# Kernel optimization log

Hardware: AMD Instinct MI355X
Metric: run time of the kernel (lower is better)

The kernel has to match this reference:

```python
import jax, jax.numpy as jnp
import numpy as np

N_NODES = 100000
N_EDGES = 1000000
N_GRAPHS = 128
IN_DIM, HID, LAT, N_LAYERS = 32, 64, 32, 3


def setup_inputs() -> dict:
    key = jax.random.key(0)
    ks = jax.random.split(key, 10)
    x = jax.random.normal(ks[0], (N_NODES, IN_DIM), dtype=jnp.float32)
    edge_index = jax.random.randint(ks[1], (2, N_EDGES), 0, N_NODES, dtype=jnp.int64)
    batch = jnp.sort(jax.random.randint(ks[2], (N_NODES,), 0, N_GRAPHS, dtype=jnp.int64))
    s_in = 1.0 / np.sqrt(IN_DIM)
    s_h = 1.0 / np.sqrt(HID)
    return {
        "x": x,
        "edge_index": edge_index,
        "batch": batch,
        "w_in": jax.random.normal(ks[3], (IN_DIM, HID), dtype=jnp.float32) * s_in,
        "b_in": jnp.zeros((HID,), jnp.float32),
        "w1": jax.random.normal(ks[4], (N_LAYERS, HID, HID), dtype=jnp.float32) * s_h,
        "b1": jnp.zeros((N_LAYERS, HID), jnp.float32),
        "w2": jax.random.normal(ks[5], (N_LAYERS, HID, HID), dtype=jnp.float32) * s_h,
        "b2": jnp.zeros((N_LAYERS, HID), jnp.float32),
        "w_fc": jax.random.normal(ks[6], (HID, LAT), dtype=jnp.float32) * s_h,
        "b_fc": jnp.zeros((LAT,), jnp.float32),
    }


def reference(x, edge_index, batch, w_in, b_in, w1, b1, w2, b2, w_fc, b_fc):
    # Input projection: [N, in] -> [N, H]
    h = x @ w_in + b_in
    src, dst = edge_index[0], edge_index[1]
    for i in range(N_LAYERS):
        h_skip = h
        # GINConv (eps=0): aggregate neighbor sum then MLP
        agg = jax.ops.segment_sum(h[src], dst, num_segments=N_NODES)  # [N, H]
        m = h + agg
        m = jax.nn.relu(m @ w1[i] + b1[i])
        m = jax.nn.relu(m @ w2[i] + b2[i])
        # dropout is identity in eval mode; residual skip
        h = m + h_skip
    # global_add_pool over graphs
    pooled = jax.ops.segment_sum(h, batch, num_segments=N_GRAPHS)  # [G, H]
    return pooled @ w_fc + b_fc
```

## Files before the change

kernel.cpp:

```cpp
#include <hip/hip_runtime.h>

#define N_NODES 100000
#define N_EDGES 1000000
#define N_GRAPHS 128
#define IN_DIM 32
#define HID 64
#define LAT 32
#define N_LAYERS 3

#define MPAD 68
#define NB_SUM ((N_NODES + 255) / 256)

__global__ __launch_bounds__(256) void proj_kernel(
    const float* __restrict__ x, const float* __restrict__ w_in,
    const float* __restrict__ b_in, float* __restrict__ h) {
    __shared__ float ws[IN_DIM * HID];
    __shared__ float xs[4 * IN_DIM];
    int tid = threadIdx.x;
    for (int i = tid; i < IN_DIM * HID / 4; i += 256)
        ((float4*)ws)[i] = ((const float4*)w_in)[i];
    if (tid < 32) {
        int r = tid >> 3, c4 = tid & 7;
        int nn = blockIdx.x * 4 + r;
        float4 v = make_float4(0.f, 0.f, 0.f, 0.f);
        if (nn < N_NODES) v = ((const float4*)(x + (size_t)nn * IN_DIM))[c4];
        ((float4*)xs)[tid] = v;
    }
    __syncthreads();
    int w = tid >> 6, j = tid & 63;
    int n = blockIdx.x * 4 + w;
    if (n >= N_NODES) return;
    float acc = b_in[j];
#pragma unroll
    for (int k = 0; k < IN_DIM; k += 4) {
        float4 xv = *(const float4*)&xs[w * IN_DIM + k];
        acc += xv.x * ws[(k + 0) * HID + j];
        acc += xv.y * ws[(k + 1) * HID + j];
        acc += xv.z * ws[(k + 2) * HID + j];
        acc += xv.w * ws[(k + 3) * HID + j];
    }
    h[(size_t)n * HID + j] = acc;
}

__global__ __launch_bounds__(256) void hist_kernel(const int* __restrict__ ei,
                                                   int* __restrict__ counts) {
    int e = blockIdx.x * 256 + threadIdx.x;
    if (e < N_EDGES) atomicAdd(&counts[ei[N_EDGES + e]], 1);
}

__global__ __launch_bounds__(256) void block_sum_kernel(
    const int* __restrict__ counts, int* __restrict__ bsums) {
    __shared__ int sd[4];
    int i = blockIdx.x * 256 + threadIdx.x;
    int v = (i < N_NODES) ? counts[i] : 0;
#pragma unroll
    for (int off = 32; off >= 1; off >>= 1) v += __shfl_down(v, off);
    int lane = threadIdx.x & 63, w = threadIdx.x >> 6;
    if (lane == 0) sd[w] = v;
    __syncthreads();
    if (threadIdx.x == 0) bsums[blockIdx.x] = sd[0] + sd[1] + sd[2] + sd[3];
}

__global__ __launch_bounds__(256) void scan_bsums_kernel(
    const int* __restrict__ bsums, int* __restrict__ bofs, int nb) {
    __shared__ int tmp[256];
    __shared__ int carry;
    int tid = threadIdx.x;
    if (tid == 0) carry = 0;
    __syncthreads();
    for (int base = 0; base < nb; base += 256) {
        int v = (base + tid < nb) ? bsums[base + tid] : 0;
        tmp[tid] = v;
        __syncthreads();
        for (int off = 1; off < 256; off <<= 1) {
            int t = (tid >= off) ? tmp[tid - off] : 0;
            __syncthreads();
            tmp[tid] += t;
            __syncthreads();
        }
        if (base + tid < nb) bofs[base + tid] = carry + tmp[tid] - v;
        __syncthreads();
        if (tid == 255) carry += tmp[255];
        __syncthreads();
    }
}

__global__ __launch_bounds__(256) void offsets_kernel(
    const int* __restrict__ counts, const int* __restrict__ bofs,
    int* __restrict__ offsets, int* __restrict__ cursor) {
    __shared__ int tmp[256];
    int tid = threadIdx.x;
    int i = blockIdx.x * 256 + tid;
    int v = (i < N_NODES) ? counts[i] : 0;
    tmp[tid] = v;
    __syncthreads();
    for (int off = 1; off < 256; off <<= 1) {
        int t = (tid >= off) ? tmp[tid - off] : 0;
        __syncthreads();
        tmp[tid] += t;
        __syncthreads();
    }
    int excl = tmp[tid] - v + bofs[blockIdx.x];
    if (i < N_NODES) {
        offsets[i] = excl;
        cursor[i] = excl;
        if (i == N_NODES - 1) offsets[N_NODES] = excl + v;
    }
}

__global__ __launch_bounds__(256) void fill_kernel(const int* __restrict__ ei,
                                                   int* __restrict__ cursor,
                                                   int* __restrict__ srcs) {
    int e = blockIdx.x * 256 + threadIdx.x;
    if (e < N_EDGES) {
        int d = ei[N_EDGES + e];
        int p = atomicAdd(&cursor[d], 1);
        srcs[p] = ei[e];
    }
}

__global__ __launch_bounds__(256) void gather_kernel(
    const int* __restrict__ offsets, const int* __restrict__ srcs,
    const float* __restrict__ h, float* __restrict__ agg) {
    int w = threadIdx.x >> 6, j = threadIdx.x & 63;
    int n = blockIdx.x * 4 + w;
    if (n >= N_NODES) return;
    int beg = offsets[n], end = offsets[n + 1];
    float acc0 = 0.f, acc1 = 0.f, acc2 = 0.f, acc3 = 0.f;
    for (int c = beg; c < end; c += 64) {
        int myS = (c + j < end) ? srcs[c + j] : 0;
        int m = min(64, end - c);
        int i = 0;
        for (; i + 3 < m; i += 4) {
            int s0 = __shfl(myS, i);
            int s1 = __shfl(myS, i + 1);
            int s2 = __shfl(myS, i + 2);
            int s3 = __shfl(myS, i + 3);
            acc0 += h[(size_t)s0 * HID + j];
            acc1 += h[(size_t)s1 * HID + j];
            acc2 += h[(size_t)s2 * HID + j];
            acc3 += h[(size_t)s3 * HID + j];
        }
        for (; i < m; i++) acc0 += h[(size_t)__shfl(myS, i) * HID + j];
    }
    agg[(size_t)n * HID + j] = acc0 + acc1 + acc2 + acc3;
}

__global__ __launch_bounds__(512) void mlp_kernel(
    float* __restrict__ h, const float* __restrict__ agg,
    const float* __restrict__ w1, const float* __restrict__ b1,
    const float* __restrict__ w2, const float* __restrict__ b2) {
    __shared__ float w1s[HID * HID];
    __shared__ float w2s[HID * HID];
    __shared__ float ms[64 * MPAD];
    int tid = threadIdx.x;
    int row0 = blockIdx.x * 64;
    for (int i = tid; i < HID * HID / 4; i += 512) {
        ((float4*)w1s)[i] = ((const float4*)w1)[i];
        ((float4*)w2s)[i] = ((const float4*)w2)[i];
    }
#pragma unroll
    for (int i = 0; i < 2; i++) {
        int f = tid + i * 512;
        int r = f >> 4, c4 = f & 15;
        int n = row0 + r;
        float4 mv = make_float4(0.f, 0.f, 0.f, 0.f);
        if (n < N_NODES) {
            float4 h4 = ((const float4*)(h + (size_t)n * HID))[c4];
            float4 a4 = ((const float4*)(agg + (size_t)n * HID))[c4];
            mv = make_float4(h4.x + a4.x, h4.y + a4.y, h4.z + a4.z, h4.w + a4.w);
        }
        *(float4*)&ms[r * MPAD + c4 * 4] = mv;
    }
    __syncthreads();

    int ty = tid >> 4, tx = tid & 15;
    int r0 = ty * 2, c0 = tx * 4;

    float4 a0, a1;
#define GEMM_LDS(WS)                                                          \
    do {                                                                      \
        a0 = make_float4(0.f, 0.f, 0.f, 0.f); a1 = a0;                        \
        _Pragma("unroll 4")                                                   \
        for (int k0 = 0; k0 < HID; k0 += 4) {                                 \
            float4 m0 = *(const float4*)&ms[(r0 + 0) * MPAD + k0];            \
            float4 m1 = *(const float4*)&ms[(r0 + 1) * MPAD + k0];            \
            float4 w0 = *(const float4*)&WS[(k0 + 0) * HID + c0];             \
            float4 w1v = *(const float4*)&WS[(k0 + 1) * HID + c0];            \
            float4 w2v = *(const float4*)&WS[(k0 + 2) * HID + c0];            \
            float4 w3v = *(const float4*)&WS[(k0 + 3) * HID + c0];            \
            a0.x += m0.x * w0.x + m0.y * w1v.x + m0.z * w2v.x + m0.w * w3v.x; \
            a0.y += m0.x * w0.y + m0.y * w1v.y + m0.z * w2v.y + m0.w * w3v.y; \
            a0.z += m0.x * w0.z + m0.y * w1v.z + m0.z * w2v.z + m0.w * w3v.z; \
            a0.w += m0.x * w0.w + m0.y * w1v.w + m0.z * w2v.w + m0.w * w3v.w; \
            a1.x += m1.x * w0.x + m1.y * w1v.x + m1.z * w2v.x + m1.w * w3v.x; \
            a1.y += m1.x * w0.y + m1.y * w1v.y + m1.z * w2v.y + m1.w * w3v.y; \
            a1.z += m1.x * w0.z + m1.y * w1v.z + m1.z * w2v.z + m1.w * w3v.z; \
            a1.w += m1.x * w0.w + m1.y * w1v.w + m1.z * w2v.w + m1.w * w3v.w; \
        }                                                                     \
    } while (0)

    GEMM_LDS(w1s);

    float4 bv1 = *(const float4*)&b1[c0];
    float4 t0 = make_float4(fmaxf(a0.x + bv1.x, 0.f), fmaxf(a0.y + bv1.y, 0.f),
                            fmaxf(a0.z + bv1.z, 0.f), fmaxf(a0.w + bv1.w, 0.f));
    float4 t1 = make_float4(fmaxf(a1.x + bv1.x, 0.f), fmaxf(a1.y + bv1.y, 0.f),
                            fmaxf(a1.z + bv1.z, 0.f), fmaxf(a1.w + bv1.w, 0.f));

    __syncthreads();
    *(float4*)&ms[(r0 + 0) * MPAD + c0] = t0;
    *(float4*)&ms[(r0 + 1) * MPAD + c0] = t1;
    __syncthreads();

    GEMM_LDS(w2s);

    float4 bv2 = *(const float4*)&b2[c0];
#pragma unroll
    for (int i = 0; i < 2; i++) {
        int n = row0 + r0 + i;
        if (n < N_NODES) {
            float4 av = (i == 0) ? a0 : a1;
            float4 hold = *(const float4*)(h + (size_t)n * HID + c0);
            float4 o;
            o.x = fmaxf(av.x + bv2.x, 0.f) + hold.x;
            o.y = fmaxf(av.y + bv2.y, 0.f) + hold.y;
            o.z = fmaxf(av.z + bv2.z, 0.f) + hold.z;
            o.w = fmaxf(av.w + bv2.w, 0.f) + hold.w;
            *(float4*)(h + (size_t)n * HID + c0) = o;
        }
    }
#undef GEMM_LDS
}

__global__ __launch_bounds__(256) void pool_kernel(
    const float* __restrict__ h, const int* __restrict__ batch,
    float* __restrict__ pooled) {
    int tid = threadIdx.x;
    int w = tid >> 6, j = tid & 63;
    int n0 = blockIdx.x * 256 + w * 64;
    if (n0 >= N_NODES) return;
    int nend = min(n0 + 64, N_NODES);
    float acc = 0.f;
    int cur = batch[n0];
    for (int n = n0; n < nend; n++) {
        int b = batch[n];
        if (b != cur) {
            atomicAdd(&pooled[cur * HID + j], acc);
            acc = 0.f;
            cur = b;
        }
        acc += h[(size_t)n * HID + j];
    }
    atomicAdd(&pooled[cur * HID + j], acc);
}

__global__ __launch_bounds__(256) void final_kernel(
    const float* __restrict__ pooled, const float* __restrict__ w_fc,
    const float* __restrict__ b_fc, float* __restrict__ out) {
    int gid = blockIdx.x * 256 + threadIdx.x;
    if (gid >= N_GRAPHS * LAT) return;
    int g = gid >> 5, j = gid & 31;
    float acc = b_fc[j];
#pragma unroll
    for (int k = 0; k < HID; k++)
        acc += pooled[g * HID + k] * w_fc[k * LAT + j];
    out[gid] = acc;
}

extern "C" void kernel_launch(void* const* d_in, const int* in_sizes, int n_in,
                              void* d_out, int out_size, void* d_ws,
                              size_t ws_size, hipStream_t stream) {
    const float* x     = (const float*)d_in[0];
    const int*   ei    = (const int*)d_in[1];
    const int*   batch = (const int*)d_in[2];
    const float* w_in  = (const float*)d_in[3];
    const float* b_in  = (const float*)d_in[4];
    const float* w1    = (const float*)d_in[5];
    const float* b1    = (const float*)d_in[6];
    const float* w2    = (const float*)d_in[7];
    const float* b2    = (const float*)d_in[8];
    const float* w_fc  = (const float*)d_in[9];
    const float* b_fc  = (const float*)d_in[10];
    float* out = (float*)d_out;

    float* h       = (float*)d_ws;
    float* agg     = h + (size_t)N_NODES * HID;
    float* pooled  = agg + (size_t)N_NODES * HID;
    int*   offsets = (int*)(pooled + N_GRAPHS * HID);
    int*   srcs    = offsets + (N_NODES + 2);
    int* counts = (int*)agg;
    int* cursor = counts + N_NODES;
    int* bsums  = cursor + N_NODES;
    int* bofs   = bsums + (NB_SUM + 1);

    proj_kernel<<<(N_NODES + 3) / 4, 256, 0, stream>>>(x, w_in, b_in, h);

    hipMemsetAsync(counts, 0, N_NODES * sizeof(int), stream);
    hist_kernel<<<(N_EDGES + 255) / 256, 256, 0, stream>>>(ei, counts);
    block_sum_kernel<<<NB_SUM, 256, 0, stream>>>(counts, bsums);
    scan_bsums_kernel<<<1, 256, 0, stream>>>(bsums, bofs, NB_SUM);
    offsets_kernel<<<NB_SUM, 256, 0, stream>>>(counts, bofs, offsets, cursor);
    fill_kernel<<<(N_EDGES + 255) / 256, 256, 0, stream>>>(ei, cursor, srcs);

    for (int i = 0; i < N_LAYERS; i++) {
        gather_kernel<<<(N_NODES + 3) / 4, 256, 0, stream>>>(offsets, srcs, h, agg);
        mlp_kernel<<<(N_NODES + 63) / 64, 512, 0, stream>>>(
            h, agg, w1 + (size_t)i * HID * HID, b1 + (size_t)i * HID,
            w2 + (size_t)i * HID * HID, b2 + (size_t)i * HID);
    }

    hipMemsetAsync(pooled, 0, N_GRAPHS * HID * sizeof(float), stream);
    pool_kernel<<<(N_NODES + 255) / 256, 256, 0, stream>>>(h, batch, pooled);
    final_kernel<<<(N_GRAPHS * LAT + 255) / 256, 256, 0, stream>>>(
        pooled, w_fc, b_fc, out);
}
```

Baseline: 489.8 us.

## Fuse gather into MLP kernel and store node features in bf16

Merges the per-layer neighbor gather and MLP into one kernel, so the aggregate array is no longer written to and read back from global memory. Node features are kept in bf16 with ping-pong buffers, halving gather traffic, and the fill kernel uses a nontemporal store. In exchange, bf16 storage adds rounding error that compounds over three residual layers. The gather now runs inside a 512-thread block with heavy LDS use, which may lower occupancy for the latency-bound gather.

```diff
diff --git a/kernel.cpp b/kernel.cpp
--- a/kernel.cpp
+++ b/kernel.cpp
@@ -11,9 +11,18 @@
 #define MPAD 68
 #define NB_SUM ((N_NODES + 255) / 256)
 
+__device__ __forceinline__ float bf2f(unsigned short u) {
+    return __uint_as_float(((unsigned int)u) << 16);
+}
+__device__ __forceinline__ unsigned short f2bf(float f) {
+    unsigned int x = __float_as_uint(f);
+    x += 0x7fffu + ((x >> 16) & 1u);
+    return (unsigned short)(x >> 16);
+}
+
 __global__ __launch_bounds__(256) void proj_kernel(
     const float* __restrict__ x, const float* __restrict__ w_in,
-    const float* __restrict__ b_in, float* __restrict__ h) {
+    const float* __restrict__ b_in, unsigned short* __restrict__ h) {
     __shared__ float ws[IN_DIM * HID];
     __shared__ float xs[4 * IN_DIM];
     int tid = threadIdx.x;
@@ -39,7 +48,7 @@
         acc += xv.z * ws[(k + 2) * HID + j];
         acc += xv.w * ws[(k + 3) * HID + j];
     }
-    h[(size_t)n * HID + j] = acc;
+    h[(size_t)n * HID + j] = f2bf(acc);
 }
 
 __global__ __launch_bounds__(256) void hist_kernel(const int* __restrict__ ei,
@@ -114,40 +123,15 @@
     int e = blockIdx.x * 256 + threadIdx.x;
     if (e < N_EDGES) {
         int d = ei[N_EDGES + e];
+        int s = ei[e];
         int p = atomicAdd(&cursor[d], 1);
-        srcs[p] = ei[e];
-    }
-}
-
-__global__ __launch_bounds__(256) void gather_kernel(
+        __builtin_nontemporal_store(s, &srcs[p]);
+    }
+}
+
+__global__ __launch_bounds__(512) void layer_kernel(
+    const unsigned short* __restrict__ h_in, unsigned short* __restrict__ h_out,
     const int* __restrict__ offsets, const int* __restrict__ srcs,
-    const float* __restrict__ h, float* __restrict__ agg) {
-    int w = threadIdx.x >> 6, j = threadIdx.x & 63;
-    int n = blockIdx.x * 4 + w;
-    if (n >= N_NODES) return;
-    int beg = offsets[n], end = offsets[n + 1];
-    float acc0 = 0.f, acc1 = 0.f, acc2 = 0.f, acc3 = 0.f;
-    for (int c = beg; c < end; c += 64) {
-        int myS = (c + j < end) ? srcs[c + j] : 0;
-        int m = min(64, end - c);
-        int i = 0;
-        for (; i + 3 < m; i += 4) {
-            int s0 = __shfl(myS, i);
-            int s1 = __shfl(myS, i + 1);
-            int s2 = __shfl(myS, i + 2);
-            int s3 = __shfl(myS, i + 3);
-            acc0 += h[(size_t)s0 * HID + j];
-            acc1 += h[(size_t)s1 * HID + j];
-            acc2 += h[(size_t)s2 * HID + j];
-            acc3 += h[(size_t)s3 * HID + j];
-        }
-        for (; i < m; i++) acc0 += h[(size_t)__shfl(myS, i) * HID + j];
-    }
-    agg[(size_t)n * HID + j] = acc0 + acc1 + acc2 + acc3;
-}
-
-__global__ __launch_bounds__(512) void mlp_kernel(
-    float* __restrict__ h, const float* __restrict__ agg,
     const float* __restrict__ w1, const float* __restrict__ b1,
     const float* __restrict__ w2, const float* __restrict__ b2) {
     __shared__ float w1s[HID * HID];
@@ -159,18 +143,33 @@
         ((float4*)w1s)[i] = ((const float4*)w1)[i];
         ((float4*)w2s)[i] = ((const float4*)w2)[i];
     }
-#pragma unroll
-    for (int i = 0; i < 2; i++) {
-        int f = tid + i * 512;
-        int r = f >> 4, c4 = f & 15;
+
+    int w = tid >> 6, j = tid & 63;
+    for (int r = w * 8; r < w * 8 + 8; r++) {
         int n = row0 + r;
-        float4 mv = make_float4(0.f, 0.f, 0.f, 0.f);
+        float acc0 = 0.f, acc1 = 0.f, acc2 = 0.f, acc3 = 0.f;
         if (n < N_NODES) {
-            float4 h4 = ((const float4*)(h + (size_t)n * HID))[c4];
-            float4 a4 = ((const float4*)(agg + (size_t)n * HID))[c4];
-            mv = make_float4(h4.x + a4.x, h4.y + a4.y, h4.z + a4.z, h4.w + a4.w);
+            int beg = offsets[n], end = offsets[n + 1];
+            for (int c = beg; c < end; c += 64) {
+                int myS = (c + j < end) ? srcs[c + j] : 0;
+                int m = min(64, end - c);
+                int i2 = 0;
+                for (; i2 + 3 < m; i2 += 4) {
+                    int s0 = __shfl(myS, i2);
+                    int s1 = __shfl(myS, i2 + 1);
+                    int s2 = __shfl(myS, i2 + 2);
+                    int s3 = __shfl(myS, i2 + 3);
+                    acc0 += bf2f(h_in[(size_t)s0 * HID + j]);
+                    acc1 += bf2f(h_in[(size_t)s1 * HID + j]);
+                    acc2 += bf2f(h_in[(size_t)s2 * HID + j]);
+                    acc3 += bf2f(h_in[(size_t)s3 * HID + j]);
+                }
+                for (; i2 < m; i2++)
+                    acc0 += bf2f(h_in[(size_t)__shfl(myS, i2) * HID + j]);
+            }
+            acc0 += acc1 + acc2 + acc3 + bf2f(h_in[(size_t)n * HID + j]);
         }
-        *(float4*)&ms[r * MPAD + c4 * 4] = mv;
+        ms[r * MPAD + j] = acc0;
     }
     __syncthreads();
 
@@ -221,20 +220,22 @@
         int n = row0 + r0 + i;
         if (n < N_NODES) {
             float4 av = (i == 0) ? a0 : a1;
-            float4 hold = *(const float4*)(h + (size_t)n * HID + c0);
-            float4 o;
-            o.x = fmaxf(av.x + bv2.x, 0.f) + hold.x;
-            o.y = fmaxf(av.y + bv2.y, 0.f) + hold.y;
-            o.z = fmaxf(av.z + bv2.z, 0.f) + hold.z;
-            o.w = fmaxf(av.w + bv2.w, 0.f) + hold.w;
-            *(float4*)(h + (size_t)n * HID + c0) = o;
+            const unsigned short* hp = h_in + (size_t)n * HID + c0;
+            float o0 = fmaxf(av.x + bv2.x, 0.f) + bf2f(hp[0]);
+            float o1 = fmaxf(av.y + bv2.y, 0.f) + bf2f(hp[1]);
+            float o2 = fmaxf(av.z + bv2.z, 0.f) + bf2f(hp[2]);
+            float o3 = fmaxf(av.w + bv2.w, 0.f) + bf2f(hp[3]);
+            uint2 pk;
+            pk.x = (unsigned int)f2bf(o0) | ((unsigned int)f2bf(o1) << 16);
+            pk.y = (unsigned int)f2bf(o2) | ((unsigned int)f2bf(o3) << 16);
+            *(uint2*)(h_out + (size_t)n * HID + c0) = pk;
         }
     }
 #undef GEMM_LDS
 }
 
 __global__ __launch_bounds__(256) void pool_kernel(
-    const float* __restrict__ h, const int* __restrict__ batch,
+    const unsigned short* __restrict__ h, const int* __restrict__ batch,
     float* __restrict__ pooled) {
     int tid = threadIdx.x;
     int w = tid >> 6, j = tid & 63;
@@ -250,7 +251,7 @@
             acc = 0.f;
             cur = b;
         }
-        acc += h[(size_t)n * HID + j];
+        acc += bf2f(h[(size_t)n * HID + j]);
     }
     atomicAdd(&pooled[cur * HID + j], acc);
 }
@@ -284,17 +285,17 @@
     const float* b_fc  = (const float*)d_in[10];
     float* out = (float*)d_out;
 
-    float* h       = (float*)d_ws;
-    float* agg     = h + (size_t)N_NODES * HID;
-    float* pooled  = agg + (size_t)N_NODES * HID;
+    unsigned short* h0 = (unsigned short*)d_ws;
+    unsigned short* h1 = h0 + (size_t)N_NODES * HID;
+    float* pooled  = (float*)(h1 + (size_t)N_NODES * HID);
     int*   offsets = (int*)(pooled + N_GRAPHS * HID);
     int*   srcs    = offsets + (N_NODES + 2);
-    int* counts = (int*)agg;
+    int* counts = (int*)h1;
     int* cursor = counts + N_NODES;
     int* bsums  = cursor + N_NODES;
     int* bofs   = bsums + (NB_SUM + 1);
 
-    proj_kernel<<<(N_NODES + 3) / 4, 256, 0, stream>>>(x, w_in, b_in, h);
+    proj_kernel<<<(N_NODES + 3) / 4, 256, 0, stream>>>(x, w_in, b_in, h0);
 
     hipMemsetAsync(counts, 0, N_NODES * sizeof(int), stream);
     hist_kernel<<<(N_EDGES + 255) / 256, 256, 0, stream>>>(ei, counts);
@@ -303,15 +304,20 @@
     offsets_kernel<<<NB_SUM, 256, 0, stream>>>(counts, bofs, offsets, cursor);
     fill_kernel<<<(N_EDGES + 255) / 256, 256, 0, stream>>>(ei, cursor, srcs);
 
+    const unsigned short* hin = h0;
+    unsigned short* hout = h1;
     for (int i = 0; i < N_LAYERS; i++) {
-        gather_kernel<<<(N_NODES + 3) / 4, 256, 0, stream>>>(offsets, srcs, h, agg);
-        mlp_kernel<<<(N_NODES + 63) / 64, 512, 0, stream>>>(
-            h, agg, w1 + (size_t)i * HID * HID, b1 + (size_t)i * HID,
+        layer_kernel<<<(N_NODES + 63) / 64, 512, 0, stream>>>(
+            hin, hout, offsets, srcs,
+            w1 + (size_t)i * HID * HID, b1 + (size_t)i * HID,
             w2 + (size_t)i * HID * HID, b2 + (size_t)i * HID);
+        const unsigned short* tmp = hout;
+        hout = (unsigned short*)hin;
+        hin = tmp;
     }
 
     hipMemsetAsync(pooled, 0, N_GRAPHS * HID * sizeof(float), stream);
-    pool_kernel<<<(N_NODES + 255) / 256, 256, 0, stream>>>(h, batch, pooled);
+    pool_kernel<<<(N_NODES + 255) / 256, 256, 0, stream>>>(hin, batch, pooled);
     final_kernel<<<(N_GRAPHS * LAT + 255) / 256, 256, 0, stream>>>(
         pooled, w_fc, b_fc, out);
 }
```

After: 572.3 us. +16.8%, slower.
